# Performance work log

Hardware: AMD Instinct MI355X
Metric: run time of the kernel (lower is better)

Reference implementation:

```python
import jax, jax.numpy as jnp
import numpy as np

B, N, K = 8, 2048, 64          # clouds, points per cloud, max neighbors
RATIO, R = 0.5, 0.2
M = int(np.ceil(RATIO * N))    # FPS samples per cloud = 1024
F = 64                         # input feature dim
C0, C1, C2 = 67, 64, 128       # local_nn channels (C0 = F + 3)
EPS = 1e-5


def setup_inputs() -> dict:
    key = jax.random.key(0)
    ks = jax.random.split(key, 8)
    x = jax.random.normal(ks[0], (B * N, F), jnp.float32)
    pos = jax.random.uniform(ks[1], (B * N, 3), jnp.float32)
    batch = jnp.repeat(jnp.arange(B, dtype=jnp.int32), N)
    W1 = jax.random.normal(ks[2], (C0, C1), jnp.float32) / np.sqrt(C0)
    b1 = jnp.zeros((C1,), jnp.float32)
    g1 = jnp.ones((C1,), jnp.float32)
    be1 = jnp.zeros((C1,), jnp.float32)
    W2 = jax.random.normal(ks[3], (C1, C2), jnp.float32) / np.sqrt(C1)
    b2 = jnp.zeros((C2,), jnp.float32)
    g2 = jnp.ones((C2,), jnp.float32)
    be2 = jnp.zeros((C2,), jnp.float32)
    return {"x": x, "pos": pos, "batch": batch, "W1": W1, "b1": b1,
            "g1": g1, "be1": be1, "W2": W2, "b2": b2, "g2": g2, "be2": be2}


def _fps_single(p):
    """Farthest point sampling on one cloud p:[N,3], start at index 0 (random_start=False)."""
    d0 = jnp.sum((p - p[0]) ** 2, axis=-1)
    def body(mind, _):
        nxt = jnp.argmax(mind)
        d = jnp.sum((p - p[nxt]) ** 2, axis=-1)
        return jnp.minimum(mind, d), nxt
    _, rest = jax.lax.scan(body, d0, None, length=M - 1)
    return jnp.concatenate([jnp.zeros((1,), rest.dtype), rest])  # [M]


def _masked_bn(h, mask, gamma, beta):
    """Training-mode BatchNorm1d over valid edges. h:[B,M,K,C], mask:[B,M,K,1]."""
    cnt = jnp.sum(mask)
    mean = jnp.sum(h * mask, axis=(0, 1, 2)) / cnt
    var = jnp.sum(mask * (h - mean) ** 2, axis=(0, 1, 2)) / cnt
    return (h - mean) * jax.lax.rsqrt(var + EPS) * gamma + beta


def _forward(x, pos, W1, b1, g1, be1, W2, b2, g2, be2):
    xb = x.reshape(B, N, F)
    pb = pos.reshape(B, N, 3)
    # --- FPS (sequential farthest point sampling, per cloud) ---
    idx_loc = jax.vmap(_fps_single)(pb)                      # [B,M] local indices
    q = jnp.take_along_axis(pb, idx_loc[..., None], axis=1)  # [B,M,3] centers
    # --- radius ball query: first K in-ball points in index order ---
    d2 = jnp.sum((q[:, :, None, :] - pb[:, None, :, :]) ** 2, axis=-1)  # [B,M,N]
    inball = d2 <= R * R
    order = jnp.argsort(jnp.logical_not(inball), axis=-1, stable=True)
    nbr = order[..., :K]                                     # [B,M,K]
    valid = jnp.take_along_axis(inball, nbr, axis=-1)        # [B,M,K] bool
    vm = valid[..., None].astype(x.dtype)
    # --- gather -> local_nn MLP -> masked max scatter (PointConv) ---
    bidx = jnp.arange(B)[:, None, None]
    x_src = xb[bidx, nbr]                                    # [B,M,K,F]
    p_src = pb[bidx, nbr]                                    # [B,M,K,3]
    h = jnp.concatenate([x_src, p_src - q[:, :, None, :]], axis=-1)  # [B,M,K,C0]
    h = jax.nn.relu(jnp.einsum('bmkc,cd->bmkd', h, W1) + b1)
    h = _masked_bn(h, vm, g1, be1)
    h = jax.nn.relu(jnp.einsum('bmkc,cd->bmkd', h, W2) + b2)
    h = _masked_bn(h, vm, g2, be2)
    neg_inf = jnp.asarray(-jnp.inf, h.dtype)
    out = jnp.max(jnp.where(valid[..., None], h, neg_inf), axis=2)   # [B,M,C2]
    x_out = out.reshape(B * M, C2)
    pos_out = q.reshape(B * M, 3)
    batch_out = jnp.repeat(jnp.arange(B, dtype=jnp.int32), M)
    idx_glob = (idx_loc + jnp.arange(B)[:, None] * N).reshape(-1)
    return x_out, pos_out, batch_out, idx_glob


def reference(x, pos, batch, W1, b1, g1, be1, W2, b2, g2, be2):
    # `batch` is assumed to be uniform: B clouds of N points each (as built in setup_inputs).
    return _forward(x, pos, W1, b1, g1, be1, W2, b2, g2, be2)
```

## Files before the change

kernel.cpp:

```cpp
#include <hip/hip_runtime.h>
#include <math.h>

#define Bc   8
#define Nc   2048
#define Mc   1024
#define Kc   64
#define Fc   64
#define C0c  67
#define C1c  64
#define C2c  128
#define NGRP (Bc*Mc)
#define R2c  0.04f
#define EPSc 1e-5f
#define NBLK 2048
#define GPB  (NGRP/NBLK)
#define FPSB 8
#define MAXW 2040

__device__ __forceinline__ float d2nf(float dx, float dy, float dz) {
  return __fadd_rn(__fadd_rn(__fmul_rn(dx,dx), __fmul_rn(dy,dy)), __fmul_rn(dz,dz));
}

__device__ __forceinline__ void fma4(float* a, float h, const float4 w) {
  a[0] = fmaf(h, w.x, a[0]); a[1] = fmaf(h, w.y, a[1]);
  a[2] = fmaf(h, w.z, a[2]); a[3] = fmaf(h, w.w, a[3]);
}

template<int CTRL>
__device__ __forceinline__ float dpp_maxf(float x) {
  const int o = __builtin_amdgcn_update_dpp(0, __float_as_int(x), CTRL, 0xf, 0xf, true);
  return fmaxf(x, __int_as_float(o));
}
__device__ __forceinline__ float wave_max64(float x) {
  x = dpp_maxf<0x111>(x);
  x = dpp_maxf<0x112>(x);
  x = dpp_maxf<0x114>(x);
  x = dpp_maxf<0x118>(x);
  x = dpp_maxf<0x142>(x);
  x = dpp_maxf<0x143>(x);
  return __int_as_float(__builtin_amdgcn_readlane(__float_as_int(x), 63));
}

union FusedSh {
  struct {
    __align__(16) float sV[2][4];
    __align__(16) float sI[2][4];
    __align__(16) float sX[2][4];
    __align__(16) float sY[2][4];
    __align__(16) float sZ[2][4];
  } f;
  struct {
    __align__(16) float inb[Kc][68];
    int   sc[256];
    int   snbr[Kc];
    int   sli;
    float sred[C1c], sqred[C1c];
  } w;
};

__global__ __launch_bounds__(256) void k_clear(unsigned long long* __restrict__ pub64,
                                               int* __restrict__ cnt_total) {
  const int i = blockIdx.x*256 + threadIdx.x;
  if (i < Bc*256) pub64[i] = 0ull;
  if (i == 0) *cnt_total = 0;
}

__global__ __launch_bounds__(256, 4) void k_fused(
    const float* __restrict__ pos, const float* __restrict__ x,
    const float* __restrict__ W1, const float* __restrict__ b1,
    unsigned long long* __restrict__ pub64,
    int* __restrict__ nbr, int* __restrict__ cntarr, float* __restrict__ q_ws,
    int* __restrict__ cnt_total,
    float* __restrict__ out_pos, float* __restrict__ out_batch, float* __restrict__ out_idx,
    float* __restrict__ p1sum, float* __restrict__ p1sq, int nworkers)
{
  __shared__ FusedSh sh;
  const int t = threadIdx.x;

  if (blockIdx.x < FPSB) {
    __builtin_amdgcn_s_setprio(3);
    const int b = blockIdx.x;
    const float* pb = pos + (size_t)b*Nc*3;
    const int base = t*8;
    float X[8],Y[8],Z[8],Mv[8];
    {
      float4 buf[6];
      const float4* src = (const float4*)(pb + (size_t)base*3);
      #pragma unroll
      for (int ii=0; ii<6; ii++) buf[ii] = src[ii];
      const float* pf = (const float*)buf;
      #pragma unroll
      for (int i=0;i<8;i++){ X[i]=pf[i*3+0]; Y[i]=pf[i*3+1]; Z[i]=pf[i*3+2]; }
    }
    const float q0x=pb[0], q0y=pb[1], q0z=pb[2];
    #pragma unroll
    for (int i=0;i<8;i++) Mv[i] = d2nf(X[i]-q0x, Y[i]-q0y, Z[i]-q0z);
    float m = fmaxf(fmaxf(fmaxf(Mv[0],Mv[1]), fmaxf(Mv[2],Mv[3])),
                    fmaxf(fmaxf(Mv[4],Mv[5]), fmaxf(Mv[6],Mv[7])));
    const int wid = t >> 6, lane = t & 63;
    unsigned long long pubacc = 0ull;
    for (int sel = 1; sel < Mc; sel++) {
      const float v = wave_max64(m);
      const unsigned long long bal = __ballot(m == v);
      const int l0 = __ffsll(bal) - 1;
      int fpos = 7;
      #pragma unroll
      for (int i=6;i>=0;i--) fpos = (Mv[i]==v) ? i : fpos;
      float sx=X[7], sy=Y[7], sz=Z[7];
      #pragma unroll
      for (int i=6;i>=0;i--){ const bool p=(Mv[i]==v); sx=p?X[i]:sx; sy=p?Y[i]:sy; sz=p?Z[i]:sz; }
      const int par = sel & 1;
      if (lane == l0) {
        sh.f.sV[par][wid] = v;
        sh.f.sI[par][wid] = __int_as_float(base + fpos);
        sh.f.sX[par][wid] = sx; sh.f.sY[par][wid] = sy; sh.f.sZ[par][wid] = sz;
      }
      __syncthreads();
      const float4 Vv = *(const float4*)sh.f.sV[par];
      const float4 Iv = *(const float4*)sh.f.sI[par];
      const float4 Xv = *(const float4*)sh.f.sX[par];
      const float4 Yv = *(const float4*)sh.f.sY[par];
      const float4 Zv = *(const float4*)sh.f.sZ[par];
      const float bm = fmaxf(fmaxf(Vv.x,Vv.y), fmaxf(Vv.z,Vv.w));
      int fi = __float_as_int(Iv.w);
      float nqx=Xv.w, nqy=Yv.w, nqz=Zv.w;
      if (Vv.z == bm) { fi=__float_as_int(Iv.z); nqx=Xv.z; nqy=Yv.z; nqz=Zv.z; }
      if (Vv.y == bm) { fi=__float_as_int(Iv.y); nqx=Xv.y; nqy=Yv.y; nqz=Zv.y; }
      if (Vv.x == bm) { fi=__float_as_int(Iv.x); nqx=Xv.x; nqy=Yv.x; nqz=Zv.x; }
      pubacc |= ((unsigned long long)(unsigned)fi) << (11*(sel&3));
      if ((sel & 3) == 3) {
        if (t == 0)
          __hip_atomic_store(&pub64[b*256 + (sel>>2)], pubacc | (1ull<<63),
                             __ATOMIC_RELAXED, __HIP_MEMORY_SCOPE_AGENT);
        pubacc = 0ull;
      }
      #pragma unroll
      for (int i=0;i<8;i++) {
        const float d = d2nf(X[i]-nqx, Y[i]-nqy, Z[i]-nqz);
        Mv[i] = fminf(Mv[i], d);
      }
      m = fmaxf(fmaxf(fmaxf(Mv[0],Mv[1]), fmaxf(Mv[2],Mv[3])),
                fmaxf(fmaxf(Mv[4],Mv[5]), fmaxf(Mv[6],Mv[7])));
    }
  } else {
    const int w = blockIdx.x - FPSB;
    const int c0 = (t & 15) * 4, kg = t >> 4;
    const int gk = t >> 2, gq = t & 3;
    const float4 b1q = *(const float4*)(b1 + c0);
    float ssum0=0,ssum1=0,ssum2=0,ssum3=0, ssq0=0,ssq1=0,ssq2=0,ssq3=0;
    for (int kk = w; kk < NGRP; kk += nworkers) {
      const int s = kk >> 3, b = kk & 7;
      const int g = b*Mc + s;
      if (t == 0) {
        unsigned long long v;
        while (!((v = __hip_atomic_load(&pub64[b*256 + (s>>2)],
                                        __ATOMIC_RELAXED, __HIP_MEMORY_SCOPE_AGENT)) >> 63))
          __builtin_amdgcn_s_sleep(8);
        sh.w.sli = (int)((v >> (11*(s&3))) & 0x7FFull);
      }
      __syncthreads();
      const int li = sh.w.sli;
      const float* pb = pos + (size_t)b*Nc*3;
      const float qx = pb[li*3+0], qy = pb[li*3+1], qz = pb[li*3+2];
      const int base = t*8;
      unsigned mask = 0;
      #pragma unroll
      for (int i=0;i<8;i++){
        const int j = base+i;
        const float d = d2nf(pb[j*3+0]-qx, pb[j*3+1]-qy, pb[j*3+2]-qz);
        if (d <= R2c) mask |= (1u<<i);
      }
      const int c = __popc(mask);
      sh.w.sc[t] = c; __syncthreads();
      for (int off=1; off<256; off<<=1) {
        const int add = (t>=off) ? sh.w.sc[t-off] : 0;
        __syncthreads();
        sh.w.sc[t] += add;
        __syncthreads();
      }
      const int total = sh.w.sc[255];
      int slot = sh.w.sc[t] - c;
      #pragma unroll
      for (int i=0;i<8;i++){
        if (mask & (1u<<i)) {
          if (slot < Kc) { nbr[(size_t)g*Kc + slot] = base+i; sh.w.snbr[slot] = base+i; }
          slot++;
        }
      }
      const int cnt = total < Kc ? total : Kc;
      if (t == 0) {
        cntarr[g] = cnt;
        atomicAdd(cnt_total, cnt);
        q_ws[g*4+0]=qx; q_ws[g*4+1]=qy; q_ws[g*4+2]=qz;
        out_pos[g*3+0]=qx; out_pos[g*3+1]=qy; out_pos[g*3+2]=qz;
        out_batch[g] = (float)b;
        out_idx[g]   = (float)(b*Nc + li);
      }
      __syncthreads();
      {
        float4* dst = (float4*)(&sh.w.inb[gk][0]);
        if (gk < cnt) {
          const int idx = sh.w.snbr[gk];
          const float4* xr = (const float4*)(x + ((size_t)b*Nc + idx)*Fc);
          #pragma unroll
          for (int ii=0; ii<4; ii++) dst[gq*4+ii] = xr[gq*4+ii];
          if (gq == 0) {
            const float* pp = pos + ((size_t)b*Nc + idx)*3;
            sh.w.inb[gk][64] = pp[0] - qx;
            sh.w.inb[gk][65] = pp[1] - qy;
            sh.w.inb[gk][66] = pp[2] - qz;
            sh.w.inb[gk][67] = 0.f;
          }
        } else {
          const float4 z4 = make_float4(0.f,0.f,0.f,0.f);
          #pragma unroll
          for (int ii=0; ii<4; ii++) dst[gq*4+ii] = z4;
          if (gq == 0) { sh.w.inb[gk][64]=0.f; sh.w.inb[gk][65]=0.f; sh.w.inb[gk][66]=0.f; sh.w.inb[gk][67]=0.f; }
        }
      }
      __syncthreads();
      float acc[4][4];
      #pragma unroll
      for (int j=0;j<4;j++){acc[j][0]=0.f;acc[j][1]=0.f;acc[j][2]=0.f;acc[j][3]=0.f;}
      for (int cq = 0; cq < 16; cq++) {
        const int cc = cq*4;
        const float4 h0 = *(const float4*)(&sh.w.inb[kg*4+0][cc]);
        const float4 h1 = *(const float4*)(&sh.w.inb[kg*4+1][cc]);
        const float4 h2 = *(const float4*)(&sh.w.inb[kg*4+2][cc]);
        const float4 h3 = *(const float4*)(&sh.w.inb[kg*4+3][cc]);
        const float4 w0 = *(const float4*)(W1 + (cc+0)*C1c + c0);
        const float4 w1 = *(const float4*)(W1 + (cc+1)*C1c + c0);
        const float4 w2 = *(const float4*)(W1 + (cc+2)*C1c + c0);
        const float4 w3 = *(const float4*)(W1 + (cc+3)*C1c + c0);
        fma4(acc[0], h0.x, w0); fma4(acc[1], h1.x, w0); fma4(acc[2], h2.x, w0); fma4(acc[3], h3.x, w0);
        fma4(acc[0], h0.y, w1); fma4(acc[1], h1.y, w1); fma4(acc[2], h2.y, w1); fma4(acc[3], h3.y, w1);
        fma4(acc[0], h0.z, w2); fma4(acc[1], h1.z, w2); fma4(acc[2], h2.z, w2); fma4(acc[3], h3.z, w2);
        fma4(acc[0], h0.w, w3); fma4(acc[1], h1.w, w3); fma4(acc[2], h2.w, w3); fma4(acc[3], h3.w, w3);
      }
      #pragma unroll
      for (int cc = 64; cc < C0c; cc++) {
        const float4 wv = *(const float4*)(W1 + cc*C1c + c0);
        #pragma unroll
        for (int j=0;j<4;j++) fma4(acc[j], sh.w.inb[kg*4 + j][cc], wv);
      }
      #pragma unroll
      for (int j=0;j<4;j++) {
        const int k2 = kg*4 + j;
        if (k2 < cnt) {
          const float r0 = fmaxf(acc[j][0] + b1q.x, 0.f);
          const float r1 = fmaxf(acc[j][1] + b1q.y, 0.f);
          const float r2 = fmaxf(acc[j][2] + b1q.z, 0.f);
          const float r3 = fmaxf(acc[j][3] + b1q.w, 0.f);
          ssum0 += r0; ssq0 += r0*r0;
          ssum1 += r1; ssq1 += r1*r1;
          ssum2 += r2; ssq2 += r2*r2;
          ssum3 += r3; ssq3 += r3*r3;
        }
      }
      __syncthreads();
    }
    if (t < C1c) { sh.w.sred[t]=0.f; sh.w.sqred[t]=0.f; }
    __syncthreads();
    atomicAdd(&sh.w.sred[c0+0], ssum0); atomicAdd(&sh.w.sqred[c0+0], ssq0);
    atomicAdd(&sh.w.sred[c0+1], ssum1); atomicAdd(&sh.w.sqred[c0+1], ssq1);
    atomicAdd(&sh.w.sred[c0+2], ssum2); atomicAdd(&sh.w.sqred[c0+2], ssq2);
    atomicAdd(&sh.w.sred[c0+3], ssum3); atomicAdd(&sh.w.sqred[c0+3], ssq3);
    __syncthreads();
    if (t < C1c) { p1sum[(size_t)w*C1c + t] = sh.w.sred[t]; p1sq[(size_t)w*C1c + t] = sh.w.sqred[t]; }
  }
}

__global__ __launch_bounds__(256) void k_fin(const float* __restrict__ psum, const float* __restrict__ psq,
                                             const int* __restrict__ cnt_total,
                                             const float* __restrict__ gam, const float* __restrict__ bet,
                                             float* __restrict__ ac, int nch, int nparts) {
  __shared__ float rs[256], rq[256];
  const int c = blockIdx.x, t = threadIdx.x;
  float s = 0.f, sq = 0.f;
  for (int p = t; p < nparts; p += 256) { s += psum[(size_t)p*nch + c]; sq += psq[(size_t)p*nch + c]; }
  rs[t] = s; rq[t] = sq; __syncthreads();
  for (int off = 128; off > 0; off >>= 1) {
    if (t < off) { rs[t] += rs[t+off]; rq[t] += rq[t+off]; }
    __syncthreads();
  }
  if (t == 0) {
    const float cntf = (float)(*cnt_total);
    const float mean = rs[0] / cntf;
    const float var = fmaxf(rq[0] / cntf - mean*mean, 0.f);
    const float a = gam[c] / sqrtf(var + EPSc);
    ac[c] = a;
    ac[nch + c] = bet[c] - mean * a;
  }
}

__global__ __launch_bounds__(256) void k_l2(const float* __restrict__ x, const float* __restrict__ pos,
                                            const float* __restrict__ W1, const float* __restrict__ b1,
                                            const float* __restrict__ W2, const float* __restrict__ b2,
                                            const int* __restrict__ nbr, const int* __restrict__ cntarr,
                                            const float* __restrict__ q_ws, const float* __restrict__ a1c,
                                            float* __restrict__ p2sum, float* __restrict__ p2sq,
                                            float* __restrict__ maxv) {
  __shared__ __align__(16) float inb[Kc][68];
  __shared__ __align__(16) float h1b[Kc][68];
  __shared__ float redmax[8][C2c];
  __shared__ float sred[C2c], sqred[C2c];
  const int t = threadIdx.x;
  const int c0a = (t & 15) * 4, kga = t >> 4;
  const int c0b = (t & 31) * 4, kgb = t >> 5;
  const float4 b1q = *(const float4*)(b1 + c0a);
  const float4 a1q = *(const float4*)(a1c + c0a);
  const float4 c1q = *(const float4*)(a1c + C1c + c0a);
  const float4 b2q = *(const float4*)(b2 + c0b);
  float ssum0=0,ssum1=0,ssum2=0,ssum3=0, ssq0=0,ssq1=0,ssq2=0,ssq3=0;
  const int gk = t >> 2, gq = t & 3;
  for (int gi = 0; gi < GPB; gi++) {
    const int g = blockIdx.x * GPB + gi;
    const int cnt = cntarr[g];
    const int b = g >> 10;
    {
      float4* dst = (float4*)(&inb[gk][0]);
      if (gk < cnt) {
        const int idx = nbr[(size_t)g*Kc + gk];
        const float4* xr = (const float4*)(x + ((size_t)b*Nc + idx)*Fc);
        #pragma unroll
        for (int ii=0; ii<4; ii++) dst[gq*4+ii] = xr[gq*4+ii];
        if (gq == 0) {
          const float* pp = pos + ((size_t)b*Nc + idx)*3;
          inb[gk][64] = pp[0] - q_ws[g*4+0];
          inb[gk][65] = pp[1] - q_ws[g*4+1];
          inb[gk][66] = pp[2] - q_ws[g*4+2];
          inb[gk][67] = 0.f;
        }
      } else {
        const float4 z4 = make_float4(0.f,0.f,0.f,0.f);
        #pragma unroll
        for (int ii=0; ii<4; ii++) dst[gq*4+ii] = z4;
        if (gq == 0) { inb[gk][64]=0.f; inb[gk][65]=0.f; inb[gk][66]=0.f; inb[gk][67]=0.f; }
      }
    }
    __syncthreads();
    {
      float acc[4][4];
      #pragma unroll
      for (int j=0;j<4;j++){acc[j][0]=0.f;acc[j][1]=0.f;acc[j][2]=0.f;acc[j][3]=0.f;}
      for (int cq = 0; cq < 16; cq++) {
        const int cc = cq*4;
        const float4 h0 = *(const float4*)(&inb[kga*4+0][cc]);
        const float4 h1 = *(const float4*)(&inb[kga*4+1][cc]);
        const float4 h2 = *(const float4*)(&inb[kga*4+2][cc]);
        const float4 h3 = *(const float4*)(&inb[kga*4+3][cc]);
        const float4 w0 = *(const float4*)(W1 + (cc+0)*C1c + c0a);
        const float4 w1 = *(const float4*)(W1 + (cc+1)*C1c + c0a);
        const float4 w2 = *(const float4*)(W1 + (cc+2)*C1c + c0a);
        const float4 w3 = *(const float4*)(W1 + (cc+3)*C1c + c0a);
        fma4(acc[0], h0.x, w0); fma4(acc[1], h1.x, w0); fma4(acc[2], h2.x, w0); fma4(acc[3], h3.x, w0);
        fma4(acc[0], h0.y, w1); fma4(acc[1], h1.y, w1); fma4(acc[2], h2.y, w1); fma4(acc[3], h3.y, w1);
        fma4(acc[0], h0.z, w2); fma4(acc[1], h1.z, w2); fma4(acc[2], h2.z, w2); fma4(acc[3], h3.z, w2);
        fma4(acc[0], h0.w, w3); fma4(acc[1], h1.w, w3); fma4(acc[2], h2.w, w3); fma4(acc[3], h3.w, w3);
      }
      #pragma unroll
      for (int cc = 64; cc < C0c; cc++) {
        const float4 w = *(const float4*)(W1 + cc*C1c + c0a);
        #pragma unroll
        for (int j=0;j<4;j++) fma4(acc[j], inb[kga*4 + j][cc], w);
      }
      #pragma unroll
      for (int j=0;j<4;j++) {
        const int k = kga*4 + j;
        float4 h;
        h.x = a1q.x * fmaxf(acc[j][0] + b1q.x, 0.f) + c1q.x;
        h.y = a1q.y * fmaxf(acc[j][1] + b1q.y, 0.f) + c1q.y;
        h.z = a1q.z * fmaxf(acc[j][2] + b1q.z, 0.f) + c1q.z;
        h.w = a1q.w * fmaxf(acc[j][3] + b1q.w, 0.f) + c1q.w;
        *(float4*)(&h1b[k][c0a]) = h;
      }
    }
    __syncthreads();
    {
      float acc[8][4];
      #pragma unroll
      for (int j=0;j<8;j++){acc[j][0]=0.f;acc[j][1]=0.f;acc[j][2]=0.f;acc[j][3]=0.f;}
      for (int cq = 0; cq < 16; cq++) {
        const int cc = cq*4;
        float4 hb[8];
        #pragma unroll
        for (int j=0;j<8;j++) hb[j] = *(const float4*)(&h1b[kgb*8+j][cc]);
        const float4 w0 = *(const float4*)(W2 + (cc+0)*C2c + c0b);
        const float4 w1 = *(const float4*)(W2 + (cc+1)*C2c + c0b);
        const float4 w2 = *(const float4*)(W2 + (cc+2)*C2c + c0b);
        const float4 w3 = *(const float4*)(W2 + (cc+3)*C2c + c0b);
        #pragma unroll
        for (int j=0;j<8;j++) {
          fma4(acc[j], hb[j].x, w0);
          fma4(acc[j], hb[j].y, w1);
          fma4(acc[j], hb[j].z, w2);
          fma4(acc[j], hb[j].w, w3);
        }
      }
      float lx0=-INFINITY,lx1=-INFINITY,lx2=-INFINITY,lx3=-INFINITY;
      #pragma unroll
      for (int j=0;j<8;j++) {
        const int k = kgb*8 + j;
        if (k < cnt) {
          const float r0 = fmaxf(acc[j][0] + b2q.x, 0.f);
          const float r1 = fmaxf(acc[j][1] + b2q.y, 0.f);
          const float r2 = fmaxf(acc[j][2] + b2q.z, 0.f);
          const float r3 = fmaxf(acc[j][3] + b2q.w, 0.f);
          ssum0 += r0; ssq0 += r0*r0;
          ssum1 += r1; ssq1 += r1*r1;
          ssum2 += r2; ssq2 += r2*r2;
          ssum3 += r3; ssq3 += r3*r3;
          lx0 = fmaxf(lx0, r0);
          lx1 = fmaxf(lx1, r1);
          lx2 = fmaxf(lx2, r2);
          lx3 = fmaxf(lx3, r3);
        }
      }
      redmax[kgb][c0b+0]=lx0; redmax[kgb][c0b+1]=lx1; redmax[kgb][c0b+2]=lx2; redmax[kgb][c0b+3]=lx3;
    }
    __syncthreads();
    if (t < C2c) {
      float mx = redmax[0][t];
      #pragma unroll
      for (int w=1; w<8; w++) mx = fmaxf(mx, redmax[w][t]);
      maxv[(size_t)g*C2c + t] = mx;
    }
    __syncthreads();
  }
  if (t < C2c) { sred[t] = 0.f; sqred[t] = 0.f; }
  __syncthreads();
  atomicAdd(&sred[c0b+0], ssum0); atomicAdd(&sqred[c0b+0], ssq0);
  atomicAdd(&sred[c0b+1], ssum1); atomicAdd(&sqred[c0b+1], ssq1);
  atomicAdd(&sred[c0b+2], ssum2); atomicAdd(&sqred[c0b+2], ssq2);
  atomicAdd(&sred[c0b+3], ssum3); atomicAdd(&sqred[c0b+3], ssq3);
  __syncthreads();
  if (t < C2c) { p2sum[(size_t)blockIdx.x*C2c + t] = sred[t]; p2sq[(size_t)blockIdx.x*C2c + t] = sqred[t]; }
}

__global__ __launch_bounds__(256) void k_out(const float* __restrict__ maxv,
                                             const float* __restrict__ a2c, float* __restrict__ xout) {
  const int i = blockIdx.x*256 + threadIdx.x;
  const int c = i & (C2c-1);
  xout[i] = a2c[c] * maxv[i] + a2c[C2c + c];
}

extern "C" void kernel_launch(void* const* d_in, const int* in_sizes, int n_in,
                              void* d_out, int out_size, void* d_ws, size_t ws_size,
                              hipStream_t stream) {
  (void)in_sizes; (void)n_in; (void)out_size; (void)ws_size;
  const float* x   = (const float*)d_in[0];
  const float* pos = (const float*)d_in[1];
  const float* W1  = (const float*)d_in[3];
  const float* b1  = (const float*)d_in[4];
  const float* g1  = (const float*)d_in[5];
  const float* be1 = (const float*)d_in[6];
  const float* W2  = (const float*)d_in[7];
  const float* b2  = (const float*)d_in[8];
  const float* g2  = (const float*)d_in[9];
  const float* be2 = (const float*)d_in[10];

  char* ws = (char*)d_ws;
  unsigned long long* pub64 = (unsigned long long*)(ws + 0);
  int*   cntarr    = (int*)  (ws + 32768);
  int*   nbr       = (int*)  (ws + 65536);
  float* q_ws      = (float*)(ws + 2162688);
  int*   cnt_total = (int*)  (ws + 2293760);
  float* p1sum     = (float*)(ws + 2294016);
  float* p1sq      = (float*)(ws + 2818304);
  float* p2sum     = (float*)(ws + 3342592);
  float* p2sq      = (float*)(ws + 4391168);
  float* a1c       = (float*)(ws + 5439744);
  float* a2c       = (float*)(ws + 5440256);
  float* maxv      = (float*)(ws + 5441280);

  float* xout      = (float*)d_out;
  float* out_pos   = xout + (size_t)NGRP*C2c;
  float* out_batch = out_pos + (size_t)NGRP*3;
  float* out_idx   = out_batch + NGRP;

  static int g_W = 0;
  if (g_W == 0) {
    int nb = 0;
    if (hipOccupancyMaxActiveBlocksPerMultiprocessor(&nb, reinterpret_cast<const void*>(k_fused),
                                                     256, 0) != hipSuccess || nb < 1) nb = 4;
    hipDeviceProp_t prop;
    int mp = 256;
    if (hipGetDeviceProperties(&prop, 0) == hipSuccess && prop.multiProcessorCount > 0)
      mp = prop.multiProcessorCount;
    int wv = nb * mp - FPSB;
    if (wv > MAXW) wv = MAXW;
    if (wv < 8)    wv = 8;
    g_W = wv;
  }
  const int nw = g_W;

  k_clear<<<FPSB, 256, 0, stream>>>(pub64, cnt_total);
  k_fused<<<FPSB + nw, 256, 0, stream>>>(pos, x, W1, b1, pub64, nbr, cntarr, q_ws,
                                         cnt_total, out_pos, out_batch, out_idx,
                                         p1sum, p1sq, nw);
  k_fin<<<C1c, 256, 0, stream>>>(p1sum, p1sq, cnt_total, g1, be1, a1c, C1c, nw);
  k_l2<<<NBLK, 256, 0, stream>>>(x, pos, W1, b1, W2, b2, nbr, cntarr, q_ws, a1c,
                                 p2sum, p2sq, maxv);
  k_fin<<<C2c, 256, 0, stream>>>(p2sum, p2sq, cnt_total, g2, be2, a2c, C2c, NBLK);
  k_out<<<(NGRP*C2c)/256, 256, 0, stream>>>(maxv, a2c, xout);
}
```

Baseline: 793.0 us.

## Merge all stages into one persistent kernel with software grid barriers

Folds the BN-statistics finalize, second MLP layer and output affine kernels into the persistent fused kernel. Stages are separated by atomic-counter grid barriers, and per-block partials are reduced straight into global atomics instead of partial arrays plus separate reduction kernels. This removes four kernel launches and their gaps. In exchange, every block must be co-resident for the barriers to work, the larger shared union may lower occupancy, and float atomic accumulation makes the sums nondeterministic.

```diff
diff --git a/kernel.cpp b/kernel.cpp
--- a/kernel.cpp
+++ b/kernel.cpp
@@ -12,10 +12,20 @@
 #define NGRP (Bc*Mc)
 #define R2c  0.04f
 #define EPSc 1e-5f
-#define NBLK 2048
-#define GPB  (NGRP/NBLK)
 #define FPSB 8
-#define MAXW 2040
+
+#define WS_PUB      0
+#define WS_BAR      16384
+#define WS_CNT      16400
+#define WS_G1SUM    16640
+#define WS_G1SQ     16896
+#define WS_G2SUM    17152
+#define WS_G2SQ     17664
+#define WS_ZERO_QW  2304
+#define WS_CNTARR   32768
+#define WS_NBR      65536
+#define WS_QWS      2162688
+#define WS_MAXV     2293760
 
 __device__ __forceinline__ float d2nf(float dx, float dy, float dz) {
   return __fadd_rn(__fadd_rn(__fmul_rn(dx,dx), __fmul_rn(dy,dy)), __fmul_rn(dz,dz));
@@ -41,7 +51,19 @@
   return __int_as_float(__builtin_amdgcn_readlane(__float_as_int(x), 63));
 }
 
-union FusedSh {
+__device__ __forceinline__ void gbar(int* __restrict__ ctr, int target) {
+  __syncthreads();
+  if (threadIdx.x == 0) {
+    __threadfence();
+    __hip_atomic_fetch_add(ctr, 1, __ATOMIC_RELEASE, __HIP_MEMORY_SCOPE_AGENT);
+    while (__hip_atomic_load(ctr, __ATOMIC_ACQUIRE, __HIP_MEMORY_SCOPE_AGENT) < target)
+      __builtin_amdgcn_s_sleep(8);
+    __threadfence();
+  }
+  __syncthreads();
+}
+
+union MegaSh {
   struct {
     __align__(16) float sV[2][4];
     __align__(16) float sI[2][4];
@@ -56,25 +78,36 @@
     int   sli;
     float sred[C1c], sqred[C1c];
   } w;
+  struct {
+    __align__(16) float inb[Kc][68];
+    __align__(16) float h1b[Kc][68];
+    float redmax[8][C2c];
+    float sred[C2c], sqred[C2c];
+    __align__(16) float affs[2][C1c];
+  } l;
 };
 
-__global__ __launch_bounds__(256) void k_clear(unsigned long long* __restrict__ pub64,
-                                               int* __restrict__ cnt_total) {
-  const int i = blockIdx.x*256 + threadIdx.x;
-  if (i < Bc*256) pub64[i] = 0ull;
-  if (i == 0) *cnt_total = 0;
-}
-
-__global__ __launch_bounds__(256, 4) void k_fused(
+__global__ __launch_bounds__(256) void k_clear(unsigned long long* __restrict__ ws0) {
+  for (int i = blockIdx.x*256 + threadIdx.x; i < WS_ZERO_QW; i += gridDim.x*256)
+    ws0[i] = 0ull;
+}
+
+__global__ __launch_bounds__(256, 4) void k_mega(
     const float* __restrict__ pos, const float* __restrict__ x,
     const float* __restrict__ W1, const float* __restrict__ b1,
-    unsigned long long* __restrict__ pub64,
+    const float* __restrict__ g1, const float* __restrict__ be1,
+    const float* __restrict__ W2, const float* __restrict__ b2,
+    const float* __restrict__ g2, const float* __restrict__ be2,
+    unsigned long long* __restrict__ pub64, int* __restrict__ barctr,
+    int* __restrict__ cnt_total,
+    float* __restrict__ g1sum, float* __restrict__ g1sq,
+    float* __restrict__ g2sum, float* __restrict__ g2sq,
     int* __restrict__ nbr, int* __restrict__ cntarr, float* __restrict__ q_ws,
-    int* __restrict__ cnt_total,
-    float* __restrict__ out_pos, float* __restrict__ out_batch, float* __restrict__ out_idx,
-    float* __restrict__ p1sum, float* __restrict__ p1sq, int nworkers)
+    float* __restrict__ maxv,
+    float* __restrict__ xout, float* __restrict__ out_pos,
+    float* __restrict__ out_batch, float* __restrict__ out_idx, int T)
 {
-  __shared__ FusedSh sh;
+  __shared__ MegaSh sh;
   const int t = threadIdx.x;
 
   if (blockIdx.x < FPSB) {
@@ -142,8 +175,10 @@
       m = fmaxf(fmaxf(fmaxf(Mv[0],Mv[1]), fmaxf(Mv[2],Mv[3])),
                 fmaxf(fmaxf(Mv[4],Mv[5]), fmaxf(Mv[6],Mv[7])));
     }
+    __builtin_amdgcn_s_setprio(0);
   } else {
     const int w = blockIdx.x - FPSB;
+    const int nworkers = T - FPSB;
     const int c0 = (t & 15) * 4, kg = t >> 4;
     const int gk = t >> 2, gq = t & 3;
     const float4 b1q = *(const float4*)(b1 + c0);
@@ -266,182 +301,174 @@
     atomicAdd(&sh.w.sred[c0+2], ssum2); atomicAdd(&sh.w.sqred[c0+2], ssq2);
     atomicAdd(&sh.w.sred[c0+3], ssum3); atomicAdd(&sh.w.sqred[c0+3], ssq3);
     __syncthreads();
-    if (t < C1c) { p1sum[(size_t)w*C1c + t] = sh.w.sred[t]; p1sq[(size_t)w*C1c + t] = sh.w.sqred[t]; }
-  }
-}
-
-__global__ __launch_bounds__(256) void k_fin(const float* __restrict__ psum, const float* __restrict__ psq,
-                                             const int* __restrict__ cnt_total,
-                                             const float* __restrict__ gam, const float* __restrict__ bet,
-                                             float* __restrict__ ac, int nch, int nparts) {
-  __shared__ float rs[256], rq[256];
-  const int c = blockIdx.x, t = threadIdx.x;
-  float s = 0.f, sq = 0.f;
-  for (int p = t; p < nparts; p += 256) { s += psum[(size_t)p*nch + c]; sq += psq[(size_t)p*nch + c]; }
-  rs[t] = s; rq[t] = sq; __syncthreads();
-  for (int off = 128; off > 0; off >>= 1) {
-    if (t < off) { rs[t] += rs[t+off]; rq[t] += rq[t+off]; }
+    if (t < C1c) { atomicAdd(g1sum + t, sh.w.sred[t]); atomicAdd(g1sq + t, sh.w.sqred[t]); }
+  }
+
+  gbar(&barctr[0], T);
+
+  if (t < C1c) {
+    const float s  = __hip_atomic_load(g1sum + t, __ATOMIC_RELAXED, __HIP_MEMORY_SCOPE_AGENT);
+    const float sq = __hip_atomic_load(g1sq  + t, __ATOMIC_RELAXED, __HIP_MEMORY_SCOPE_AGENT);
+    const float cntf = (float)__hip_atomic_load(cnt_total, __ATOMIC_RELAXED, __HIP_MEMORY_SCOPE_AGENT);
+    const float mean = s / cntf;
+    const float var = fmaxf(sq / cntf - mean*mean, 0.f);
+    const float a = g1[t] / sqrtf(var + EPSc);
+    sh.l.affs[0][t] = a;
+    sh.l.affs[1][t] = be1[t] - mean * a;
+  }
+  __syncthreads();
+
+  {
+    const int c0a = (t & 15) * 4, kga = t >> 4;
+    const int c0b = (t & 31) * 4, kgb = t >> 5;
+    const float4 b1q = *(const float4*)(b1 + c0a);
+    const float4 a1q = *(const float4*)(&sh.l.affs[0][c0a]);
+    const float4 c1q = *(const float4*)(&sh.l.affs[1][c0a]);
+    const float4 b2q = *(const float4*)(b2 + c0b);
+    float ssum0=0,ssum1=0,ssum2=0,ssum3=0, ssq0=0,ssq1=0,ssq2=0,ssq3=0;
+    const int gk = t >> 2, gq = t & 3;
+    for (int g = blockIdx.x; g < NGRP; g += T) {
+      const int cnt = cntarr[g];
+      const int b = g >> 10;
+      {
+        float4* dst = (float4*)(&sh.l.inb[gk][0]);
+        if (gk < cnt) {
+          const int idx = nbr[(size_t)g*Kc + gk];
+          const float4* xr = (const float4*)(x + ((size_t)b*Nc + idx)*Fc);
+          #pragma unroll
+          for (int ii=0; ii<4; ii++) dst[gq*4+ii] = xr[gq*4+ii];
+          if (gq == 0) {
+            const float* pp = pos + ((size_t)b*Nc + idx)*3;
+            sh.l.inb[gk][64] = pp[0] - q_ws[g*4+0];
+            sh.l.inb[gk][65] = pp[1] - q_ws[g*4+1];
+            sh.l.inb[gk][66] = pp[2] - q_ws[g*4+2];
+            sh.l.inb[gk][67] = 0.f;
+          }
+        } else {
+          const float4 z4 = make_float4(0.f,0.f,0.f,0.f);
+          #pragma unroll
+          for (int ii=0; ii<4; ii++) dst[gq*4+ii] = z4;
+          if (gq == 0) { sh.l.inb[gk][64]=0.f; sh.l.inb[gk][65]=0.f; sh.l.inb[gk][66]=0.f; sh.l.inb[gk][67]=0.f; }
+        }
+      }
+      __syncthreads();
+      {
+        float acc[4][4];
+        #pragma unroll
+        for (int j=0;j<4;j++){acc[j][0]=0.f;acc[j][1]=0.f;acc[j][2]=0.f;acc[j][3]=0.f;}
+        for (int cq = 0; cq < 16; cq++) {
+          const int cc = cq*4;
+          const float4 h0 = *(const float4*)(&sh.l.inb[kga*4+0][cc]);
+          const float4 h1 = *(const float4*)(&sh.l.inb[kga*4+1][cc]);
+          const float4 h2 = *(const float4*)(&sh.l.inb[kga*4+2][cc]);
+          const float4 h3 = *(const float4*)(&sh.l.inb[kga*4+3][cc]);
+          const float4 w0 = *(const float4*)(W1 + (cc+0)*C1c + c0a);
+          const float4 w1 = *(const float4*)(W1 + (cc+1)*C1c + c0a);
+          const float4 w2 = *(const float4*)(W1 + (cc+2)*C1c + c0a);
+          const float4 w3 = *(const float4*)(W1 + (cc+3)*C1c + c0a);
+          fma4(acc[0], h0.x, w0); fma4(acc[1], h1.x, w0); fma4(acc[2], h2.x, w0); fma4(acc[3], h3.x, w0);
+          fma4(acc[0], h0.y, w1); fma4(acc[1], h1.y, w1); fma4(acc[2], h2.y, w1); fma4(acc[3], h3.y, w1);
+          fma4(acc[0], h0.z, w2); fma4(acc[1], h1.z, w2); fma4(acc[2], h2.z, w2); fma4(acc[3], h3.z, w2);
+          fma4(acc[0], h0.w, w3); fma4(acc[1], h1.w, w3); fma4(acc[2], h2.w, w3); fma4(acc[3], h3.w, w3);
+        }
+        #pragma unroll
+        for (int cc = 64; cc < C0c; cc++) {
+          const float4 wv = *(const float4*)(W1 + cc*C1c + c0a);
+          #pragma unroll
+          for (int j=0;j<4;j++) fma4(acc[j], sh.l.inb[kga*4 + j][cc], wv);
+        }
+        #pragma unroll
+        for (int j=0;j<4;j++) {
+          const int k = kga*4 + j;
+          float4 h;
+          h.x = a1q.x * fmaxf(acc[j][0] + b1q.x, 0.f) + c1q.x;
+          h.y = a1q.y * fmaxf(acc[j][1] + b1q.y, 0.f) + c1q.y;
+          h.z = a1q.z * fmaxf(acc[j][2] + b1q.z, 0.f) + c1q.z;
+          h.w = a1q.w * fmaxf(acc[j][3] + b1q.w, 0.f) + c1q.w;
+          *(float4*)(&sh.l.h1b[k][c0a]) = h;
+        }
+      }
+      __syncthreads();
+      {
+        float acc[8][4];
+        #pragma unroll
+        for (int j=0;j<8;j++){acc[j][0]=0.f;acc[j][1]=0.f;acc[j][2]=0.f;acc[j][3]=0.f;}
+        for (int cq = 0; cq < 16; cq++) {
+          const int cc = cq*4;
+          float4 hb[8];
+          #pragma unroll
+          for (int j=0;j<8;j++) hb[j] = *(const float4*)(&sh.l.h1b[kgb*8+j][cc]);
+          const float4 w0 = *(const float4*)(W2 + (cc+0)*C2c + c0b);
+          const float4 w1 = *(const float4*)(W2 + (cc+1)*C2c + c0b);
+          const float4 w2 = *(const float4*)(W2 + (cc+2)*C2c + c0b);
+          const float4 w3 = *(const float4*)(W2 + (cc+3)*C2c + c0b);
+          #pragma unroll
+          for (int j=0;j<8;j++) {
+            fma4(acc[j], hb[j].x, w0);
+            fma4(acc[j], hb[j].y, w1);
+            fma4(acc[j], hb[j].z, w2);
+            fma4(acc[j], hb[j].w, w3);
+          }
+        }
+        float lx0=-INFINITY,lx1=-INFINITY,lx2=-INFINITY,lx3=-INFINITY;
+        #pragma unroll
+        for (int j=0;j<8;j++) {
+          const int k = kgb*8 + j;
+          if (k < cnt) {
+            const float r0 = fmaxf(acc[j][0] + b2q.x, 0.f);
+            const float r1 = fmaxf(acc[j][1] + b2q.y, 0.f);
+            const float r2 = fmaxf(acc[j][2] + b2q.z, 0.f);
+            const float r3 = fmaxf(acc[j][3] + b2q.w, 0.f);
+            ssum0 += r0; ssq0 += r0*r0;
+            ssum1 += r1; ssq1 += r1*r1;
+            ssum2 += r2; ssq2 += r2*r2;
+            ssum3 += r3; ssq3 += r3*r3;
+            lx0 = fmaxf(lx0, r0);
+            lx1 = fmaxf(lx1, r1);
+            lx2 = fmaxf(lx2, r2);
+            lx3 = fmaxf(lx3, r3);
+          }
+        }
+        sh.l.redmax[kgb][c0b+0]=lx0; sh.l.redmax[kgb][c0b+1]=lx1;
+        sh.l.redmax[kgb][c0b+2]=lx2; sh.l.redmax[kgb][c0b+3]=lx3;
+      }
+      __syncthreads();
+      if (t < C2c) {
+        float mx = sh.l.redmax[0][t];
+        #pragma unroll
+        for (int w2i=1; w2i<8; w2i++) mx = fmaxf(mx, sh.l.redmax[w2i][t]);
+        maxv[(size_t)g*C2c + t] = mx;
+      }
+      __syncthreads();
+    }
+    if (t < C2c) { sh.l.sred[t] = 0.f; sh.l.sqred[t] = 0.f; }
     __syncthreads();
-  }
-  if (t == 0) {
-    const float cntf = (float)(*cnt_total);
-    const float mean = rs[0] / cntf;
-    const float var = fmaxf(rq[0] / cntf - mean*mean, 0.f);
-    const float a = gam[c] / sqrtf(var + EPSc);
-    ac[c] = a;
-    ac[nch + c] = bet[c] - mean * a;
-  }
-}
-
-__global__ __launch_bounds__(256) void k_l2(const float* __restrict__ x, const float* __restrict__ pos,
-                                            const float* __restrict__ W1, const float* __restrict__ b1,
-                                            const float* __restrict__ W2, const float* __restrict__ b2,
-                                            const int* __restrict__ nbr, const int* __restrict__ cntarr,
-                                            const float* __restrict__ q_ws, const float* __restrict__ a1c,
-                                            float* __restrict__ p2sum, float* __restrict__ p2sq,
-                                            float* __restrict__ maxv) {
-  __shared__ __align__(16) float inb[Kc][68];
-  __shared__ __align__(16) float h1b[Kc][68];
-  __shared__ float redmax[8][C2c];
-  __shared__ float sred[C2c], sqred[C2c];
-  const int t = threadIdx.x;
-  const int c0a = (t & 15) * 4, kga = t >> 4;
-  const int c0b = (t & 31) * 4, kgb = t >> 5;
-  const float4 b1q = *(const float4*)(b1 + c0a);
-  const float4 a1q = *(const float4*)(a1c + c0a);
-  const float4 c1q = *(const float4*)(a1c + C1c + c0a);
-  const float4 b2q = *(const float4*)(b2 + c0b);
-  float ssum0=0,ssum1=0,ssum2=0,ssum3=0, ssq0=0,ssq1=0,ssq2=0,ssq3=0;
-  const int gk = t >> 2, gq = t & 3;
-  for (int gi = 0; gi < GPB; gi++) {
-    const int g = blockIdx.x * GPB + gi;
-    const int cnt = cntarr[g];
-    const int b = g >> 10;
-    {
-      float4* dst = (float4*)(&inb[gk][0]);
-      if (gk < cnt) {
-        const int idx = nbr[(size_t)g*Kc + gk];
-        const float4* xr = (const float4*)(x + ((size_t)b*Nc + idx)*Fc);
-        #pragma unroll
-        for (int ii=0; ii<4; ii++) dst[gq*4+ii] = xr[gq*4+ii];
-        if (gq == 0) {
-          const float* pp = pos + ((size_t)b*Nc + idx)*3;
-          inb[gk][64] = pp[0] - q_ws[g*4+0];
-          inb[gk][65] = pp[1] - q_ws[g*4+1];
-          inb[gk][66] = pp[2] - q_ws[g*4+2];
-          inb[gk][67] = 0.f;
-        }
-      } else {
-        const float4 z4 = make_float4(0.f,0.f,0.f,0.f);
-        #pragma unroll
-        for (int ii=0; ii<4; ii++) dst[gq*4+ii] = z4;
-        if (gq == 0) { inb[gk][64]=0.f; inb[gk][65]=0.f; inb[gk][66]=0.f; inb[gk][67]=0.f; }
-      }
-    }
+    atomicAdd(&sh.l.sred[c0b+0], ssum0); atomicAdd(&sh.l.sqred[c0b+0], ssq0);
+    atomicAdd(&sh.l.sred[c0b+1], ssum1); atomicAdd(&sh.l.sqred[c0b+1], ssq1);
+    atomicAdd(&sh.l.sred[c0b+2], ssum2); atomicAdd(&sh.l.sqred[c0b+2], ssq2);
+    atomicAdd(&sh.l.sred[c0b+3], ssum3); atomicAdd(&sh.l.sqred[c0b+3], ssq3);
     __syncthreads();
-    {
-      float acc[4][4];
-      #pragma unroll
-      for (int j=0;j<4;j++){acc[j][0]=0.f;acc[j][1]=0.f;acc[j][2]=0.f;acc[j][3]=0.f;}
-      for (int cq = 0; cq < 16; cq++) {
-        const int cc = cq*4;
-        const float4 h0 = *(const float4*)(&inb[kga*4+0][cc]);
-        const float4 h1 = *(const float4*)(&inb[kga*4+1][cc]);
-        const float4 h2 = *(const float4*)(&inb[kga*4+2][cc]);
-        const float4 h3 = *(const float4*)(&inb[kga*4+3][cc]);
-        const float4 w0 = *(const float4*)(W1 + (cc+0)*C1c + c0a);
-        const float4 w1 = *(const float4*)(W1 + (cc+1)*C1c + c0a);
-        const float4 w2 = *(const float4*)(W1 + (cc+2)*C1c + c0a);
-        const float4 w3 = *(const float4*)(W1 + (cc+3)*C1c + c0a);
-        fma4(acc[0], h0.x, w0); fma4(acc[1], h1.x, w0); fma4(acc[2], h2.x, w0); fma4(acc[3], h3.x, w0);
-        fma4(acc[0], h0.y, w1); fma4(acc[1], h1.y, w1); fma4(acc[2], h2.y, w1); fma4(acc[3], h3.y, w1);
-        fma4(acc[0], h0.z, w2); fma4(acc[1], h1.z, w2); fma4(acc[2], h2.z, w2); fma4(acc[3], h3.z, w2);
-        fma4(acc[0], h0.w, w3); fma4(acc[1], h1.w, w3); fma4(acc[2], h2.w, w3); fma4(acc[3], h3.w, w3);
-      }
-      #pragma unroll
-      for (int cc = 64; cc < C0c; cc++) {
-        const float4 w = *(const float4*)(W1 + cc*C1c + c0a);
-        #pragma unroll
-        for (int j=0;j<4;j++) fma4(acc[j], inb[kga*4 + j][cc], w);
-      }
-      #pragma unroll
-      for (int j=0;j<4;j++) {
-        const int k = kga*4 + j;
-        float4 h;
-        h.x = a1q.x * fmaxf(acc[j][0] + b1q.x, 0.f) + c1q.x;
-        h.y = a1q.y * fmaxf(acc[j][1] + b1q.y, 0.f) + c1q.y;
-        h.z = a1q.z * fmaxf(acc[j][2] + b1q.z, 0.f) + c1q.z;
-        h.w = a1q.w * fmaxf(acc[j][3] + b1q.w, 0.f) + c1q.w;
-        *(float4*)(&h1b[k][c0a]) = h;
-      }
-    }
-    __syncthreads();
-    {
-      float acc[8][4];
-      #pragma unroll
-      for (int j=0;j<8;j++){acc[j][0]=0.f;acc[j][1]=0.f;acc[j][2]=0.f;acc[j][3]=0.f;}
-      for (int cq = 0; cq < 16; cq++) {
-        const int cc = cq*4;
-        float4 hb[8];
-        #pragma unroll
-        for (int j=0;j<8;j++) hb[j] = *(const float4*)(&h1b[kgb*8+j][cc]);
-        const float4 w0 = *(const float4*)(W2 + (cc+0)*C2c + c0b);
-        const float4 w1 = *(const float4*)(W2 + (cc+1)*C2c + c0b);
-        const float4 w2 = *(const float4*)(W2 + (cc+2)*C2c + c0b);
-        const float4 w3 = *(const float4*)(W2 + (cc+3)*C2c + c0b);
-        #pragma unroll
-        for (int j=0;j<8;j++) {
-          fma4(acc[j], hb[j].x, w0);
-          fma4(acc[j], hb[j].y, w1);
-          fma4(acc[j], hb[j].z, w2);
-          fma4(acc[j], hb[j].w, w3);
-        }
-      }
-      float lx0=-INFINITY,lx1=-INFINITY,lx2=-INFINITY,lx3=-INFINITY;
-      #pragma unroll
-      for (int j=0;j<8;j++) {
-        const int k = kgb*8 + j;
-        if (k < cnt) {
-          const float r0 = fmaxf(acc[j][0] + b2q.x, 0.f);
-          const float r1 = fmaxf(acc[j][1] + b2q.y, 0.f);
-          const float r2 = fmaxf(acc[j][2] + b2q.z, 0.f);
-          const float r3 = fmaxf(acc[j][3] + b2q.w, 0.f);
-          ssum0 += r0; ssq0 += r0*r0;
-          ssum1 += r1; ssq1 += r1*r1;
-          ssum2 += r2; ssq2 += r2*r2;
-          ssum3 += r3; ssq3 += r3*r3;
-          lx0 = fmaxf(lx0, r0);
-          lx1 = fmaxf(lx1, r1);
-          lx2 = fmaxf(lx2, r2);
-          lx3 = fmaxf(lx3, r3);
-        }
-      }
-      redmax[kgb][c0b+0]=lx0; redmax[kgb][c0b+1]=lx1; redmax[kgb][c0b+2]=lx2; redmax[kgb][c0b+3]=lx3;
-    }
-    __syncthreads();
-    if (t < C2c) {
-      float mx = redmax[0][t];
-      #pragma unroll
-      for (int w=1; w<8; w++) mx = fmaxf(mx, redmax[w][t]);
-      maxv[(size_t)g*C2c + t] = mx;
-    }
-    __syncthreads();
-  }
-  if (t < C2c) { sred[t] = 0.f; sqred[t] = 0.f; }
+    if (t < C2c) { atomicAdd(g2sum + t, sh.l.sred[t]); atomicAdd(g2sq + t, sh.l.sqred[t]); }
+  }
+
+  gbar(&barctr[1], T);
+
+  if (t < C2c) {
+    const float s  = __hip_atomic_load(g2sum + t, __ATOMIC_RELAXED, __HIP_MEMORY_SCOPE_AGENT);
+    const float sq = __hip_atomic_load(g2sq  + t, __ATOMIC_RELAXED, __HIP_MEMORY_SCOPE_AGENT);
+    const float cntf = (float)__hip_atomic_load(cnt_total, __ATOMIC_RELAXED, __HIP_MEMORY_SCOPE_AGENT);
+    const float mean = s / cntf;
+    const float var = fmaxf(sq / cntf - mean*mean, 0.f);
+    const float a = g2[t] / sqrtf(var + EPSc);
+    sh.l.redmax[0][t] = a;
+    sh.l.redmax[1][t] = be2[t] - mean * a;
+  }
   __syncthreads();
-  atomicAdd(&sred[c0b+0], ssum0); atomicAdd(&sqred[c0b+0], ssq0);
-  atomicAdd(&sred[c0b+1], ssum1); atomicAdd(&sqred[c0b+1], ssq1);
-  atomicAdd(&sred[c0b+2], ssum2); atomicAdd(&sqred[c0b+2], ssq2);
-  atomicAdd(&sred[c0b+3], ssum3); atomicAdd(&sqred[c0b+3], ssq3);
-  __syncthreads();
-  if (t < C2c) { p2sum[(size_t)blockIdx.x*C2c + t] = sred[t]; p2sq[(size_t)blockIdx.x*C2c + t] = sqred[t]; }
-}
-
-__global__ __launch_bounds__(256) void k_out(const float* __restrict__ maxv,
-                                             const float* __restrict__ a2c, float* __restrict__ xout) {
-  const int i = blockIdx.x*256 + threadIdx.x;
-  const int c = i & (C2c-1);
-  xout[i] = a2c[c] * maxv[i] + a2c[C2c + c];
+
+  for (int i = blockIdx.x*256 + t; i < NGRP*C2c; i += T*256) {
+    const int c = i & (C2c-1);
+    xout[i] = sh.l.redmax[0][c] * maxv[i] + sh.l.redmax[1][c];
+  }
 }
 
 extern "C" void kernel_launch(void* const* d_in, const int* in_sizes, int n_in,
@@ -460,47 +487,41 @@
   const float* be2 = (const float*)d_in[10];
 
   char* ws = (char*)d_ws;
-  unsigned long long* pub64 = (unsigned long long*)(ws + 0);
-  int*   cntarr    = (int*)  (ws + 32768);
-  int*   nbr       = (int*)  (ws + 65536);
-  float* q_ws      = (float*)(ws + 2162688);
-  int*   cnt_total = (int*)  (ws + 2293760);
-  float* p1sum     = (float*)(ws + 2294016);
-  float* p1sq      = (float*)(ws + 2818304);
-  float* p2sum     = (float*)(ws + 3342592);
-  float* p2sq      = (float*)(ws + 4391168);
-  float* a1c       = (float*)(ws + 5439744);
-  float* a2c       = (float*)(ws + 5440256);
-  float* maxv      = (float*)(ws + 5441280);
+  unsigned long long* pub64 = (unsigned long long*)(ws + WS_PUB);
+  int*   barctr    = (int*)  (ws + WS_BAR);
+  int*   cnt_total = (int*)  (ws + WS_CNT);
+  float* g1sum     = (float*)(ws + WS_G1SUM);
+  float* g1sq      = (float*)(ws + WS_G1SQ);
+  float* g2sum     = (float*)(ws + WS_G2SUM);
+  float* g2sq      = (float*)(ws + WS_G2SQ);
+  int*   cntarr    = (int*)  (ws + WS_CNTARR);
+  int*   nbr       = (int*)  (ws + WS_NBR);
+  float* q_ws      = (float*)(ws + WS_QWS);
+  float* maxv      = (float*)(ws + WS_MAXV);
 
   float* xout      = (float*)d_out;
   float* out_pos   = xout + (size_t)NGRP*C2c;
   float* out_batch = out_pos + (size_t)NGRP*3;
   float* out_idx   = out_batch + NGRP;
 
-  static int g_W = 0;
-  if (g_W == 0) {
+  static int g_T = 0;
+  if (g_T == 0) {
     int nb = 0;
-    if (hipOccupancyMaxActiveBlocksPerMultiprocessor(&nb, reinterpret_cast<const void*>(k_fused),
+    if (hipOccupancyMaxActiveBlocksPerMultiprocessor(&nb, reinterpret_cast<const void*>(k_mega),
                                                      256, 0) != hipSuccess || nb < 1) nb = 4;
     hipDeviceProp_t prop;
     int mp = 256;
     if (hipGetDeviceProperties(&prop, 0) == hipSuccess && prop.multiProcessorCount > 0)
       mp = prop.multiProcessorCount;
-    int wv = nb * mp - FPSB;
-    if (wv > MAXW) wv = MAXW;
-    if (wv < 8)    wv = 8;
-    g_W = wv;
-  }
-  const int nw = g_W;
-
-  k_clear<<<FPSB, 256, 0, stream>>>(pub64, cnt_total);
-  k_fused<<<FPSB + nw, 256, 0, stream>>>(pos, x, W1, b1, pub64, nbr, cntarr, q_ws,
-                                         cnt_total, out_pos, out_batch, out_idx,
-                                         p1sum, p1sq, nw);
-  k_fin<<<C1c, 256, 0, stream>>>(p1sum, p1sq, cnt_total, g1, be1, a1c, C1c, nw);
-  k_l2<<<NBLK, 256, 0, stream>>>(x, pos, W1, b1, W2, b2, nbr, cntarr, q_ws, a1c,
-                                 p2sum, p2sq, maxv);
-  k_fin<<<C2c, 256, 0, stream>>>(p2sum, p2sq, cnt_total, g2, be2, a2c, C2c, NBLK);
-  k_out<<<(NGRP*C2c)/256, 256, 0, stream>>>(maxv, a2c, xout);
-}
+    int tv = nb * mp;
+    if (tv < FPSB + 8) tv = FPSB + 8;
+    g_T = tv;
+  }
+  const int T = g_T;
+
+  k_clear<<<8, 256, 0, stream>>>((unsigned long long*)ws);
+  k_mega<<<T, 256, 0, stream>>>(pos, x, W1, b1, g1, be1, W2, b2, g2, be2,
+                                pub64, barctr, cnt_total, g1sum, g1sq, g2sum, g2sq,
+                                nbr, cntarr, q_ws, maxv,
+                                xout, out_pos, out_batch, out_idx, T);
+}
```

Result: slower. 1.127 ms (+42.2%).

## Fold BatchNorm finalize kernels into consumers via striped atomic partial sums

Applied to the files above, without the earlier changes.

Removes the two k_fin launches. Per-block BN partial sums are now accumulated with global atomics into 8 striped slots, and each consumer block (k_l2, k_out) reduces the 8 slots and computes the affine coefficients itself. k_clear now zeroes the whole workspace header, including the partial-sum arrays. This saves two kernel launches and the strided reduction over thousands of partials, at the cost of atomic contention and redundant per-block finalize work. It also drops the MAXW clamp on the worker count.

```diff
diff --git a/kernel.cpp b/kernel.cpp
--- a/kernel.cpp
+++ b/kernel.cpp
@@ -15,7 +15,16 @@
 #define NBLK 2048
 #define GPB  (NGRP/NBLK)
 #define FPSB 8
-#define MAXW 2040
+
+#define WS_PUB      0
+#define WS_CNT      16384
+#define WS_P1PART   16640
+#define WS_P2PART   20736
+#define WS_ZERO_QW  3616
+#define WS_CNTARR   32768
+#define WS_NBR      65536
+#define WS_QWS      2162688
+#define WS_MAXV     2293760
 
 __device__ __forceinline__ float d2nf(float dx, float dy, float dz) {
   return __fadd_rn(__fadd_rn(__fmul_rn(dx,dx), __fmul_rn(dy,dy)), __fmul_rn(dz,dz));
@@ -58,11 +67,9 @@
   } w;
 };
 
-__global__ __launch_bounds__(256) void k_clear(unsigned long long* __restrict__ pub64,
-                                               int* __restrict__ cnt_total) {
-  const int i = blockIdx.x*256 + threadIdx.x;
-  if (i < Bc*256) pub64[i] = 0ull;
-  if (i == 0) *cnt_total = 0;
+__global__ __launch_bounds__(256) void k_clear(unsigned long long* __restrict__ ws0) {
+  for (int i = blockIdx.x*256 + threadIdx.x; i < WS_ZERO_QW; i += gridDim.x*256)
+    ws0[i] = 0ull;
 }
 
 __global__ __launch_bounds__(256, 4) void k_fused(
@@ -72,7 +79,7 @@
     int* __restrict__ nbr, int* __restrict__ cntarr, float* __restrict__ q_ws,
     int* __restrict__ cnt_total,
     float* __restrict__ out_pos, float* __restrict__ out_batch, float* __restrict__ out_idx,
-    float* __restrict__ p1sum, float* __restrict__ p1sq, int nworkers)
+    float* __restrict__ p1part, int nworkers)
 {
   __shared__ FusedSh sh;
   const int t = threadIdx.x;
@@ -266,30 +273,10 @@
     atomicAdd(&sh.w.sred[c0+2], ssum2); atomicAdd(&sh.w.sqred[c0+2], ssq2);
     atomicAdd(&sh.w.sred[c0+3], ssum3); atomicAdd(&sh.w.sqred[c0+3], ssq3);
     __syncthreads();
-    if (t < C1c) { p1sum[(size_t)w*C1c + t] = sh.w.sred[t]; p1sq[(size_t)w*C1c + t] = sh.w.sqred[t]; }
-  }
-}
-
-__global__ __launch_bounds__(256) void k_fin(const float* __restrict__ psum, const float* __restrict__ psq,
-                                             const int* __restrict__ cnt_total,
-                                             const float* __restrict__ gam, const float* __restrict__ bet,
-                                             float* __restrict__ ac, int nch, int nparts) {
-  __shared__ float rs[256], rq[256];
-  const int c = blockIdx.x, t = threadIdx.x;
-  float s = 0.f, sq = 0.f;
-  for (int p = t; p < nparts; p += 256) { s += psum[(size_t)p*nch + c]; sq += psq[(size_t)p*nch + c]; }
-  rs[t] = s; rq[t] = sq; __syncthreads();
-  for (int off = 128; off > 0; off >>= 1) {
-    if (t < off) { rs[t] += rs[t+off]; rq[t] += rq[t+off]; }
-    __syncthreads();
-  }
-  if (t == 0) {
-    const float cntf = (float)(*cnt_total);
-    const float mean = rs[0] / cntf;
-    const float var = fmaxf(rq[0] / cntf - mean*mean, 0.f);
-    const float a = gam[c] / sqrtf(var + EPSc);
-    ac[c] = a;
-    ac[nch + c] = bet[c] - mean * a;
+    if (t < C1c) {
+      atomicAdd(p1part + (w & 7)*C1c + t,             sh.w.sred[t]);
+      atomicAdd(p1part + 8*C1c + (w & 7)*C1c + t,     sh.w.sqred[t]);
+    }
   }
 }
 
@@ -297,19 +284,33 @@
                                             const float* __restrict__ W1, const float* __restrict__ b1,
                                             const float* __restrict__ W2, const float* __restrict__ b2,
                                             const int* __restrict__ nbr, const int* __restrict__ cntarr,
-                                            const float* __restrict__ q_ws, const float* __restrict__ a1c,
-                                            float* __restrict__ p2sum, float* __restrict__ p2sq,
-                                            float* __restrict__ maxv) {
+                                            const float* __restrict__ q_ws,
+                                            const float* __restrict__ p1part, const int* __restrict__ cnt_total,
+                                            const float* __restrict__ g1, const float* __restrict__ be1,
+                                            float* __restrict__ p2part, float* __restrict__ maxv) {
   __shared__ __align__(16) float inb[Kc][68];
   __shared__ __align__(16) float h1b[Kc][68];
   __shared__ float redmax[8][C2c];
   __shared__ float sred[C2c], sqred[C2c];
+  __shared__ __align__(16) float affs[2][C1c];
   const int t = threadIdx.x;
+  if (t < C1c) {
+    float s = 0.f, sq = 0.f;
+    #pragma unroll
+    for (int r = 0; r < 8; r++) { s += p1part[r*C1c + t]; sq += p1part[8*C1c + r*C1c + t]; }
+    const float cntf = (float)(*cnt_total);
+    const float mean = s / cntf;
+    const float var = fmaxf(sq / cntf - mean*mean, 0.f);
+    const float a = g1[t] / sqrtf(var + EPSc);
+    affs[0][t] = a;
+    affs[1][t] = be1[t] - mean * a;
+  }
+  __syncthreads();
   const int c0a = (t & 15) * 4, kga = t >> 4;
   const int c0b = (t & 31) * 4, kgb = t >> 5;
   const float4 b1q = *(const float4*)(b1 + c0a);
-  const float4 a1q = *(const float4*)(a1c + c0a);
-  const float4 c1q = *(const float4*)(a1c + C1c + c0a);
+  const float4 a1q = *(const float4*)(&affs[0][c0a]);
+  const float4 c1q = *(const float4*)(&affs[1][c0a]);
   const float4 b2q = *(const float4*)(b2 + c0b);
   float ssum0=0,ssum1=0,ssum2=0,ssum3=0, ssq0=0,ssq1=0,ssq2=0,ssq3=0;
   const int gk = t >> 2, gq = t & 3;
@@ -434,14 +435,33 @@
   atomicAdd(&sred[c0b+2], ssum2); atomicAdd(&sqred[c0b+2], ssq2);
   atomicAdd(&sred[c0b+3], ssum3); atomicAdd(&sqred[c0b+3], ssq3);
   __syncthreads();
-  if (t < C2c) { p2sum[(size_t)blockIdx.x*C2c + t] = sred[t]; p2sq[(size_t)blockIdx.x*C2c + t] = sqred[t]; }
+  if (t < C2c) {
+    atomicAdd(p2part + (blockIdx.x & 7)*C2c + t,           sred[t]);
+    atomicAdd(p2part + 8*C2c + (blockIdx.x & 7)*C2c + t,   sqred[t]);
+  }
 }
 
 __global__ __launch_bounds__(256) void k_out(const float* __restrict__ maxv,
-                                             const float* __restrict__ a2c, float* __restrict__ xout) {
-  const int i = blockIdx.x*256 + threadIdx.x;
+                                             const float* __restrict__ p2part, const int* __restrict__ cnt_total,
+                                             const float* __restrict__ g2, const float* __restrict__ be2,
+                                             float* __restrict__ xout) {
+  __shared__ float affs[2][C2c];
+  const int t = threadIdx.x;
+  if (t < C2c) {
+    float s = 0.f, sq = 0.f;
+    #pragma unroll
+    for (int r = 0; r < 8; r++) { s += p2part[r*C2c + t]; sq += p2part[8*C2c + r*C2c + t]; }
+    const float cntf = (float)(*cnt_total);
+    const float mean = s / cntf;
+    const float var = fmaxf(sq / cntf - mean*mean, 0.f);
+    const float a = g2[t] / sqrtf(var + EPSc);
+    affs[0][t] = a;
+    affs[1][t] = be2[t] - mean * a;
+  }
+  __syncthreads();
+  const int i = blockIdx.x*256 + t;
   const int c = i & (C2c-1);
-  xout[i] = a2c[c] * maxv[i] + a2c[C2c + c];
+  xout[i] = affs[0][c] * maxv[i] + affs[1][c];
 }
 
 extern "C" void kernel_launch(void* const* d_in, const int* in_sizes, int n_in,
@@ -460,18 +480,14 @@
   const float* be2 = (const float*)d_in[10];
 
   char* ws = (char*)d_ws;
-  unsigned long long* pub64 = (unsigned long long*)(ws + 0);
-  int*   cntarr    = (int*)  (ws + 32768);
-  int*   nbr       = (int*)  (ws + 65536);
-  float* q_ws      = (float*)(ws + 2162688);
-  int*   cnt_total = (int*)  (ws + 2293760);
-  float* p1sum     = (float*)(ws + 2294016);
-  float* p1sq      = (float*)(ws + 2818304);
-  float* p2sum     = (float*)(ws + 3342592);
-  float* p2sq      = (float*)(ws + 4391168);
-  float* a1c       = (float*)(ws + 5439744);
-  float* a2c       = (float*)(ws + 5440256);
-  float* maxv      = (float*)(ws + 5441280);
+  unsigned long long* pub64 = (unsigned long long*)(ws + WS_PUB);
+  int*   cnt_total = (int*)  (ws + WS_CNT);
+  float* p1part    = (float*)(ws + WS_P1PART);
+  float* p2part    = (float*)(ws + WS_P2PART);
+  int*   cntarr    = (int*)  (ws + WS_CNTARR);
+  int*   nbr       = (int*)  (ws + WS_NBR);
+  float* q_ws      = (float*)(ws + WS_QWS);
+  float* maxv      = (float*)(ws + WS_MAXV);
 
   float* xout      = (float*)d_out;
   float* out_pos   = xout + (size_t)NGRP*C2c;
@@ -488,19 +504,16 @@
     if (hipGetDeviceProperties(&prop, 0) == hipSuccess && prop.multiProcessorCount > 0)
       mp = prop.multiProcessorCount;
     int wv = nb * mp - FPSB;
-    if (wv > MAXW) wv = MAXW;
-    if (wv < 8)    wv = 8;
+    if (wv < 8) wv = 8;
     g_W = wv;
   }
   const int nw = g_W;
 
-  k_clear<<<FPSB, 256, 0, stream>>>(pub64, cnt_total);
+  k_clear<<<8, 256, 0, stream>>>((unsigned long long*)ws);
   k_fused<<<FPSB + nw, 256, 0, stream>>>(pos, x, W1, b1, pub64, nbr, cntarr, q_ws,
                                          cnt_total, out_pos, out_batch, out_idx,
-                                         p1sum, p1sq, nw);
-  k_fin<<<C1c, 256, 0, stream>>>(p1sum, p1sq, cnt_total, g1, be1, a1c, C1c, nw);
-  k_l2<<<NBLK, 256, 0, stream>>>(x, pos, W1, b1, W2, b2, nbr, cntarr, q_ws, a1c,
-                                 p2sum, p2sq, maxv);
-  k_fin<<<C2c, 256, 0, stream>>>(p2sum, p2sq, cnt_total, g2, be2, a2c, C2c, NBLK);
-  k_out<<<(NGRP*C2c)/256, 256, 0, stream>>>(maxv, a2c, xout);
-}
+                                         p1part, nw);
+  k_l2<<<NBLK, 256, 0, stream>>>(x, pos, W1, b1, W2, b2, nbr, cntarr, q_ws,
+                                 p1part, cnt_total, g1, be1, p2part, maxv);
+  k_out<<<(NGRP*C2c)/256, 256, 0, stream>>>(maxv, p2part, cnt_total, g2, be2, xout);
+}
```

Measured after the change: 795.1 us. About the same (+0.3%).
